# Kernel tuning notes

Hardware: AMD Instinct MI355X
Metric: run time of the kernel (lower is better)

The kernel has to match this reference:

```python
import jax, jax.numpy as jnp
import numpy as np

B, L, T = 32, 512, 400
EMB, PRE, ENC, ARNN, DRNN, NSYM = 512, 256, 512, 1024, 1024, 256
MEAN_COEFF, SCALE_COEFF = 1.0, 10.0


def setup_inputs() -> dict:
    key = jax.random.key(0)
    ks = jax.random.split(key, 20)
    s = 0.02
    inp = {
        'memory': jax.random.normal(ks[0], (B, L, ENC), jnp.float32),
        'decoder_inputs': jax.random.normal(ks[1], (B, EMB, T), jnp.float32),
        'memory_lengths': jax.random.randint(ks[2], (B,), L // 2, L + 1).astype(jnp.int64),
        # prenet
        'pW1': jax.random.normal(ks[3], (PRE, EMB), jnp.float32) * s,
        'pb1': jnp.zeros((PRE,), jnp.float32),
        'pW2': jax.random.normal(ks[4], (PRE, PRE), jnp.float32) * s,
        'pb2': jnp.zeros((PRE,), jnp.float32),
        # attention LSTMCell
        'aWih': jax.random.normal(ks[5], (4 * ARNN, PRE + ENC), jnp.float32) * s,
        'aWhh': jax.random.normal(ks[6], (4 * ARNN, ARNN), jnp.float32) * s,
        'abih': jnp.zeros((4 * ARNN,), jnp.float32),
        'abhh': jnp.zeros((4 * ARNN,), jnp.float32),
        # Gaussian attention param linear (weight zero-init in torch; small here)
        'attWp': jax.random.normal(ks[7], (2, ARNN), jnp.float32) * 0.001,
        'attbp': jnp.zeros((2,), jnp.float32),
        # decoder LSTMCell
        'dWih': jax.random.normal(ks[8], (4 * DRNN, ARNN + ENC), jnp.float32) * s,
        'dWhh': jax.random.normal(ks[9], (4 * DRNN, DRNN), jnp.float32) * s,
        'dbih': jnp.zeros((4 * DRNN,), jnp.float32),
        'dbhh': jnp.zeros((4 * DRNN,), jnp.float32),
        # output linear
        'oW': jax.random.normal(ks[10], (NSYM, DRNN + ENC), jnp.float32) * s,
        'ob': jnp.zeros((NSYM,), jnp.float32),
    }
    return inp


def _lstm_cell(x, h, c, Wih, Whh, bih, bhh):
    g = x @ Wih.T + bih + h @ Whh.T + bhh
    i, f, gg, o = jnp.split(g, 4, axis=-1)
    c = jax.nn.sigmoid(f) * c + jax.nn.sigmoid(i) * jnp.tanh(gg)
    h = jax.nn.sigmoid(o) * jnp.tanh(c)
    return h, c


def _decoder_core(memory, decoder_inputs, memory_lengths,
                  pW1, pb1, pW2, pb2,
                  aWih, aWhh, abih, abhh,
                  attWp, attbp,
                  dWih, dWhh, dbih, dbhh,
                  oW, ob):
    b = memory.shape[0]
    Lm = memory.shape[1]
    # go frame + time-major inputs -> prenet (dropout is identity in eval)
    x = jnp.transpose(decoder_inputs, (2, 0, 1))            # [T, B, EMB]
    x = jnp.concatenate([jnp.zeros((1, b, EMB), x.dtype), x], axis=0)  # [T+1, B, EMB]
    x = jax.nn.relu(x @ pW1.T + pb1)
    x = jax.nn.relu(x @ pW2.T + pb2)                        # [T+1, B, PRE]
    x = x[:T]                                               # loop runs T steps

    lin = jnp.arange(Lm, dtype=memory.dtype)[None, :]       # [1, L]
    pad_mask = lin >= memory_lengths[:, None].astype(memory.dtype)  # [B, L] True at pad

    def step(carry, x_t):
        ah, ac, dh, dc, ctx, mean = carry
        cell_in = jnp.concatenate([x_t, ctx], axis=1)
        ah, ac = _lstm_cell(cell_in, ah, ac, aWih, aWhh, abih, abhh)
        params = ah @ attWp.T + attbp                       # [B, 2]
        mean = mean + jnp.exp(params[:, 0:1]) * MEAN_COEFF  # [B, 1]
        scale = jnp.exp(params[:, 1:2]) * SCALE_COEFF       # [B, 1]
        Z = jnp.sqrt(2.0 * np.pi * scale ** 2)
        w = jnp.exp(-0.5 * (lin - mean) ** 2 / scale ** 2) / Z  # [B, L]
        w = jnp.where(pad_mask, 0.0, w)
        ctx = jnp.einsum('bl,bld->bd', w, memory)           # [B, ENC]
        dec_in = jnp.concatenate([ah, ctx], axis=1)
        dh, dc = _lstm_cell(dec_in, dh, dc, dWih, dWhh, dbih, dbhh)
        out = jnp.concatenate([dh, ctx], axis=1) @ oW.T + ob  # [B, NSYM]
        return (ah, ac, dh, dc, ctx, mean), (out, w, params)

    z = jnp.zeros
    carry0 = (z((b, ARNN)), z((b, ARNN)), z((b, DRNN)), z((b, DRNN)),
              z((b, ENC)), z((b, 1)))
    _, (logits, aligns, ps) = jax.lax.scan(step, carry0, x)
    # time-major -> [B, T, ...]
    return (jnp.transpose(logits, (1, 0, 2)),
            jnp.transpose(aligns, (1, 0, 2)),
            jnp.transpose(ps, (1, 0, 2)))


def reference(memory, decoder_inputs, memory_lengths,
              pW1, pb1, pW2, pb2,
              aWih, aWhh, abih, abhh,
              attWp, attbp,
              dWih, dWhh, dbih, dbhh,
              oW, ob):
    return _decoder_core(memory, decoder_inputs, memory_lengths,
                         pW1, pb1, pW2, pb2,
                         aWih, aWhh, abih, abhh,
                         attWp, attbp,
                         dWih, dWhh, dbih, dbhh,
                         oW, ob)
```

## Files before the change

### kernel.cpp

```cpp
#include <hip/hip_runtime.h>
#include <math.h>

#define Bsz   32
#define Lmem  512
#define Tsteps 400
#define EMBD  512
#define PRE   256
#define ENCD  512
#define ARNN  1024
#define DRNN  1024
#define NSYM  256

typedef _Float16 f16x8 __attribute__((ext_vector_type(8)));
typedef float    f32x4 __attribute__((ext_vector_type(4)));
typedef _Float16 half_t;

#define KA  (PRE + ENCD + ARNN)
#define KAQ (KA / 4)
#define NMA (KAQ / 32)
#define KD  (ARNN + ENCD + DRNN)
#define KDQ (KD / 4)
#define NMD (KDQ / 32)
#define LDA_A 1800
#define LDA_D 2568

__device__ __forceinline__ void st_agent_f16(half_t* p, half_t v) {
    __hip_atomic_store((unsigned short*)p, __builtin_bit_cast(unsigned short, v),
                       __ATOMIC_RELAXED, __HIP_MEMORY_SCOPE_AGENT);
}
__device__ __forceinline__ void st_agent_f32(float* p, float v) {
    __hip_atomic_store(p, v, __ATOMIC_RELAXED, __HIP_MEMORY_SCOPE_AGENT);
}
__device__ __forceinline__ void st_agent_u32(unsigned* p, unsigned v) {
    __hip_atomic_store(p, v, __ATOMIC_RELAXED, __HIP_MEMORY_SCOPE_AGENT);
}
__device__ __forceinline__ float ld_agent_f32(const float* p) {
    return __hip_atomic_load(p, __ATOMIC_RELAXED, __HIP_MEMORY_SCOPE_AGENT);
}
__device__ __forceinline__ unsigned ld_agent_u32(const unsigned* p) {
    return __hip_atomic_load(p, __ATOMIC_RELAXED, __HIP_MEMORY_SCOPE_AGENT);
}
__device__ __forceinline__ f16x8 ld_agent_f16x8(const half_t* p) {
    union { unsigned long long u[2]; f16x8 v; } c;
    c.u[0] = __hip_atomic_load((const unsigned long long*)p,
                               __ATOMIC_RELAXED, __HIP_MEMORY_SCOPE_AGENT);
    c.u[1] = __hip_atomic_load(((const unsigned long long*)p) + 1,
                               __ATOMIC_RELAXED, __HIP_MEMORY_SCOPE_AGENT);
    return c.v;
}
__device__ __forceinline__ void keep16(f16x8& v) { asm volatile("" : "+v"(v)); }

template<int KIH, int KHH>
__global__ __launch_bounds__(256) void conv_lstm_w(
    const float* __restrict__ Wih, const float* __restrict__ Whh,
    const float* __restrict__ bih, const float* __restrict__ bhh,
    half_t* __restrict__ Wcat, float* __restrict__ bsum)
{
    constexpr int K = KIH + KHH;
    const int j = blockIdx.x;
    const float* srcA = Wih + (size_t)j * KIH;
    const float* srcB = Whh + (size_t)j * KHH;
    half_t* dst = Wcat + (size_t)j * K;
    for (int k = threadIdx.x; k < KIH; k += 256) dst[k]       = (half_t)srcA[k];
    for (int k = threadIdx.x; k < KHH; k += 256) dst[KIH + k] = (half_t)srcB[k];
    if (threadIdx.x == 0) bsum[j] = bih[j] + bhh[j];
}

__global__ __launch_bounds__(256) void conv_mat(
    const float* __restrict__ src, half_t* __restrict__ dst, int n)
{
    for (int i = blockIdx.x * 256 + threadIdx.x; i < n; i += gridDim.x * 256)
        dst[i] = (half_t)src[i];
}

__global__ __launch_bounds__(256) void prenet_kernel(
    const float* __restrict__ din,
    const float* __restrict__ pW1, const float* __restrict__ pb1,
    const float* __restrict__ pW2, const float* __restrict__ pb2,
    half_t* __restrict__ xpre)
{
    __shared__ float xs[8][EMBD];
    __shared__ float h1s[8][PRE];
    const int tid = threadIdx.x;
    const int row0 = blockIdx.x * 8;

    for (int idx = tid; idx < 8 * EMBD; idx += 256) {
        int r = idx >> 9;
        int e = idx & 511;
        int rid = row0 + r;
        int t = rid >> 5;
        int b = rid & 31;
        float v = 0.f;
        if (t > 0) v = din[(size_t)b * EMBD * Tsteps + (size_t)e * Tsteps + (t - 1)];
        xs[r][e] = v;
    }
    __syncthreads();

    {
        float acc[8] = {0.f,0.f,0.f,0.f,0.f,0.f,0.f,0.f};
        const float* wr = pW1 + (size_t)tid * EMBD;
        for (int e = 0; e < EMBD; e += 4) {
            float4 wv = *(const float4*)(wr + e);
            #pragma unroll
            for (int r = 0; r < 8; ++r) {
                float4 xv = *(const float4*)&xs[r][e];
                acc[r] += wv.x * xv.x + wv.y * xv.y + wv.z * xv.z + wv.w * xv.w;
            }
        }
        float bias = pb1[tid];
        #pragma unroll
        for (int r = 0; r < 8; ++r) h1s[r][tid] = fmaxf(acc[r] + bias, 0.f);
    }
    __syncthreads();

    {
        float acc[8] = {0.f,0.f,0.f,0.f,0.f,0.f,0.f,0.f};
        const float* wr = pW2 + (size_t)tid * PRE;
        for (int e = 0; e < PRE; e += 4) {
            float4 wv = *(const float4*)(wr + e);
            #pragma unroll
            for (int r = 0; r < 8; ++r) {
                float4 xv = *(const float4*)&h1s[r][e];
                acc[r] += wv.x * xv.x + wv.y * xv.y + wv.z * xv.z + wv.w * xv.w;
            }
        }
        float bias = pb2[tid];
        #pragma unroll
        for (int r = 0; r < 8; ++r) {
            int rid = row0 + r;
            int t = rid >> 5;
            int b = rid & 31;
            xpre[(size_t)t * Bsz * PRE + (size_t)b * PRE + tid] =
                (half_t)fmaxf(acc[r] + bias, 0.f);
        }
    }
}

__device__ __forceinline__ void g_arrive(unsigned* flags, unsigned ph)
{
    asm volatile("s_waitcnt vmcnt(0)" ::: "memory");
    __syncthreads();
    if (threadIdx.x == 0)
        __hip_atomic_store(flags + blockIdx.x * 16, ph,
                           __ATOMIC_RELAXED, __HIP_MEMORY_SCOPE_AGENT);
}
__device__ __forceinline__ void g_wait(unsigned* flags, unsigned ph)
{
    if (threadIdx.x < 64) {
        const unsigned* f = flags + threadIdx.x * 64;
        for (;;) {
            unsigned a = ld_agent_u32(f);
            unsigned b = ld_agent_u32(f + 16);
            unsigned c = ld_agent_u32(f + 32);
            unsigned d = ld_agent_u32(f + 48);
            if (min(min(a, b), min(c, d)) >= ph) break;
            __builtin_amdgcn_s_sleep(2);
        }
    }
    __syncthreads();
}

__global__ __launch_bounds__(512, 1) void decoder_persistent(
    const half_t* __restrict__ Wcat_a, const float* __restrict__ bsum_a,
    const half_t* __restrict__ Wcat_d, const float* __restrict__ bsum_d,
    const half_t* __restrict__ Wo, const float* __restrict__ ob,
    const half_t* __restrict__ xpre,
    const float* __restrict__ attWp, const float* __restrict__ attbp,
    const int* __restrict__ mlen, const half_t* __restrict__ mem16,
    half_t* __restrict__ ah0, half_t* __restrict__ ah1,
    half_t* __restrict__ dh0, half_t* __restrict__ dh1,
    half_t* __restrict__ ctx0, half_t* __restrict__ ctx1,
    float* __restrict__ mean0, float* __restrict__ mean1,
    float* __restrict__ logits, float* __restrict__ aligns,
    float* __restrict__ ps,
    unsigned* flags)
{
    const int blk   = blockIdx.x;
    const int tid   = threadIdx.x;
    const int wave  = tid >> 6;
    const int lane  = tid & 63;
    const int btile = wave & 1;
    const int kq    = wave >> 1;
    const int m15   = lane & 15;
    const int kh    = lane >> 4;
    const int u0    = blk << 2;
    const int bb    = (btile << 4) + m15;

    __shared__ __align__(16) half_t wAl[16 * LDA_A];
    __shared__ __align__(16) half_t wDl[16 * LDA_D];
    __shared__ float gredA[4][2][16][16];
    __shared__ float gredD[4][2][16][16];
    __shared__ float wsh[Lmem];
    __shared__ float lred[16][33];
    __shared__ float wred8[8][2];
    __shared__ float bc2[2];

    for (int g = tid; g < 16 * (KA / 8); g += 512) {
        int r = g / (KA / 8);
        int c = (g - r * (KA / 8)) * 8;
        int jr = (r >> 2) * 1024 + u0 + (r & 3);
        *(f16x8*)(wAl + r * LDA_A + c) = *(const f16x8*)(Wcat_a + (size_t)jr * KA + c);
    }
    for (int g = tid; g < 16 * (KD / 8); g += 512) {
        int r = g / (KD / 8);
        int c = (g - r * (KD / 8)) * 8;
        int jr = (r >> 2) * 1024 + u0 + (r & 3);
        *(f16x8*)(wDl + r * LDA_D + c) = *(const f16x8*)(Wcat_d + (size_t)jr * KD + c);
    }
    float bsA[4] = {0.f,0.f,0.f,0.f}, bsD[4] = {0.f,0.f,0.f,0.f};
    float cA = 0.f, cD = 0.f;
    if (tid < 128) {
        const int ul = tid >> 5;
        #pragma unroll
        for (int gi = 0; gi < 4; ++gi) bsA[gi] = bsum_a[gi * 1024 + u0 + ul];
    } else if (tid < 256) {
        const int ul = (tid - 128) >> 5;
        #pragma unroll
        for (int gi = 0; gi < 4; ++gi) bsD[gi] = bsum_d[gi * 1024 + u0 + ul];
    }
    const half_t* lA = wAl + m15 * LDA_A + kq * KAQ + (kh << 3);
    const half_t* lD = wDl + m15 * LDA_D + kq * KDQ + (kh << 3);
    __syncthreads();

    f16x8 bvA[NMA], bvD[NMD];
    {
        const half_t* s0 = xpre;
        #pragma unroll
        for (int i = 0; i < NMA; ++i) {
            const int kg = kq * KAQ + i * 32 + (kh << 3);
            if (kg < PRE)             bvA[i] = *(const f16x8*)(s0 + bb * PRE + kg);
            else if (kg < PRE + ENCD) bvA[i] = ld_agent_f16x8(ctx1 + bb * ENCD + (kg - PRE));
            else                      bvA[i] = ld_agent_f16x8(ah1 + bb * ARNN + (kg - PRE - ENCD));
        }
    }

    unsigned ph = 0;

    for (int t = 0; t <= Tsteps; ++t) {
        const int par = t & 1;
        half_t*       ah_cur  = par ? ah1 : ah0;
        half_t*       ctx_cur = par ? ctx1 : ctx0;
        const half_t* ctx_prv = par ? ctx0 : ctx1;
        float*        mn_cur  = par ? mean1 : mean0;
        const float*  mn_prv  = par ? mean0 : mean1;
        half_t*       dh_s    = par ? dh0 : dh1;

        if (t < Tsteps) {
            f32x4 accA = {0.f,0.f,0.f,0.f};
            #pragma unroll
            for (int i = 0; i < NMA; ++i) {
                f16x8 av = *(const f16x8*)(lA + i * 32);
                accA = __builtin_amdgcn_mfma_f32_16x16x32_f16(av, bvA[i], accA, 0, 0, 0);
            }
            #pragma unroll
            for (int r = 0; r < 4; ++r)
                gredA[kq][btile][(kh << 2) + r][m15] = accA[r];
        }
        if (t > 0) {
            f32x4 accD = {0.f,0.f,0.f,0.f};
            #pragma unroll
            for (int i = 0; i < NMD; ++i) {
                f16x8 av = *(const f16x8*)(lD + i * 32);
                accD = __builtin_amdgcn_mfma_f32_16x16x32_f16(av, bvD[i], accD, 0, 0, 0);
            }
            #pragma unroll
            for (int r = 0; r < 4; ++r)
                gredD[kq][btile][(kh << 2) + r][m15] = accD[r];
        }
        __syncthreads();
        if (tid < 128) {
            if (t < Tsteps) {
                const int ul = tid >> 5;
                const int bq = tid & 31;
                const int bt = bq >> 4;
                const int nn = bq & 15;
                float g[4];
                #pragma unroll
                for (int gi = 0; gi < 4; ++gi) {
                    const int mr = (gi << 2) + ul;
                    g[gi] = gredA[0][bt][mr][nn] + gredA[1][bt][mr][nn]
                          + gredA[2][bt][mr][nn] + gredA[3][bt][mr][nn] + bsA[gi];
                }
                float si = 1.f / (1.f + expf(-g[0]));
                float sf = 1.f / (1.f + expf(-g[1]));
                float so = 1.f / (1.f + expf(-g[3]));
                cA = sf * cA + si * tanhf(g[2]);
                st_agent_f16(&ah_cur[bq * 1024 + u0 + ul], (half_t)(so * tanhf(cA)));
            }
        } else if (tid < 256) {
            if (t > 0) {
                const int lt = tid - 128;
                const int ul = lt >> 5;
                const int bq = lt & 31;
                const int bt = bq >> 4;
                const int nn = bq & 15;
                float g[4];
                #pragma unroll
                for (int gi = 0; gi < 4; ++gi) {
                    const int mr = (gi << 2) + ul;
                    g[gi] = gredD[0][bt][mr][nn] + gredD[1][bt][mr][nn]
                          + gredD[2][bt][mr][nn] + gredD[3][bt][mr][nn] + bsD[gi];
                }
                float si = 1.f / (1.f + expf(-g[0]));
                float sf = 1.f / (1.f + expf(-g[1]));
                float so = 1.f / (1.f + expf(-g[3]));
                cD = sf * cD + si * tanhf(g[2]);
                st_agent_f16(&dh_s[bq * 1024 + u0 + ul], (half_t)(so * tanhf(cD)));
            }
        }
        ++ph; g_arrive(flags, ph); g_wait(flags, ph);

        if (t < Tsteps) {
            const int abt = blk >> 3;
            const int dt  = blk & 7;
            float p0, p1;
            {
                union { unsigned u; _Float16 h[2]; } a;
                a.u = ld_agent_u32((const unsigned*)(ah_cur + abt * ARNN + 2 * tid));
                float a0 = (float)a.h[0], a1 = (float)a.h[1];
                float2 w0 = *(const float2*)(attWp + 2 * tid);
                float2 w1 = *(const float2*)(attWp + ARNN + 2 * tid);
                p0 = a0 * w0.x + a1 * w0.y;
                p1 = a0 * w1.x + a1 * w1.y;
            }
            #pragma unroll
            for (int off = 32; off > 0; off >>= 1) {
                p0 += __shfl_down(p0, off, 64);
                p1 += __shfl_down(p1, off, 64);
            }
            if (lane == 0) { wred8[wave][0] = p0; wred8[wave][1] = p1; }
            __syncthreads();
            if (tid == 0) {
                float q0 = attbp[0], q1 = attbp[1];
                #pragma unroll
                for (int w = 0; w < 8; ++w) { q0 += wred8[w][0]; q1 += wred8[w][1]; }
                float mn = ld_agent_f32(&mn_prv[abt]) + expf(q0) * 1.0f;
                float sc = expf(q1) * 10.0f;
                if (dt == 0) {
                    st_agent_f32(&mn_cur[abt], mn);
                    st_agent_f32(&ps[(size_t)abt * Tsteps * 2 + (size_t)t * 2 + 0], q0);
                    st_agent_f32(&ps[(size_t)abt * Tsteps * 2 + (size_t)t * 2 + 1], q1);
                }
                bc2[0] = mn; bc2[1] = sc;
            }
            __syncthreads();
            const float mn = bc2[0], sc = bc2[1];
            const float inv_s = 1.f / sc;
            const float coef = 0.3989422804014327f * inv_s;
            const int len = mlen[abt];
            {
                float z = ((float)tid - mn) * inv_s;
                float wv = (tid < len) ? expf(-0.5f * z * z) * coef : 0.f;
                wsh[tid] = wv;
                if (dt == 0)
                    st_agent_f32(&aligns[(size_t)abt * Tsteps * Lmem + (size_t)t * Lmem + tid], wv);
            }
            __syncthreads();
            int lo = (int)fmaxf(0.f, floorf(mn - 9.f * sc));
            int hi = (int)fminf((float)len, ceilf(mn + 9.f * sc) + 1.f);
            const int d8 = (dt << 6) + (wave << 3);
            const half_t* mb = mem16 + (size_t)abt * Lmem * ENCD + d8;
            float acc[8] = {0.f,0.f,0.f,0.f,0.f,0.f,0.f,0.f};
            for (int l = lo + lane; l < hi; l += 64) {
                f16x8 mv = *(const f16x8*)(mb + (size_t)l * ENCD);
                float w = wsh[l];
                #pragma unroll
                for (int j = 0; j < 8; ++j) acc[j] += w * (float)mv[j];
            }
            #pragma unroll
            for (int off = 32; off > 0; off >>= 1) {
                #pragma unroll
                for (int j = 0; j < 8; ++j) acc[j] += __shfl_down(acc[j], off, 64);
            }
            if (lane == 0) {
                #pragma unroll
                for (int j = 0; j < 4; ++j) {
                    union { unsigned u; _Float16 h[2]; } pk;
                    pk.h[0] = (_Float16)acc[2 * j];
                    pk.h[1] = (_Float16)acc[2 * j + 1];
                    __hip_atomic_store((unsigned*)(ctx_cur + abt * ENCD + d8 + 2 * j), pk.u,
                                       __ATOMIC_RELAXED, __HIP_MEMORY_SCOPE_AGENT);
                }
            }
        }
        if (t > 0) {
            const int b_o = tid & 31;
            const int ks  = tid >> 5;
            const half_t* wrow = Wo + (size_t)blk * (DRNN + ENCD) + ks * 96;
            float outacc = 0.f;
            #pragma unroll
            for (int half = 0; half < 2; ++half) {
                f16x8 wv[6], av[6];
                #pragma unroll
                for (int c8 = 0; c8 < 6; ++c8) {
                    const int cc = half * 6 + c8;
                    const int k = ks * 96 + cc * 8;
                    wv[c8] = *(const f16x8*)(wrow + cc * 8);
                    const half_t* ap = (k < DRNN) ? (dh_s + b_o * DRNN + k)
                                                  : (ctx_prv + b_o * ENCD + (k - DRNN));
                    av[c8] = ld_agent_f16x8(ap);
                }
                #pragma unroll
                for (int c8 = 0; c8 < 6; ++c8)
                    #pragma unroll
                    for (int e = 0; e < 8; ++e)
                        outacc += (float)wv[c8][e] * (float)av[c8][e];
            }
            lred[ks][b_o] = outacc;
            __syncthreads();
            if (tid < 32) {
                float s = 0.f;
                #pragma unroll
                for (int q = 0; q < 16; ++q) s += lred[q][tid];
                st_agent_f32(&logits[(size_t)tid * Tsteps * NSYM + (size_t)(t - 1) * NSYM + blk],
                             s + ob[blk]);
            }
        }
        if (t < Tsteps) {
            ++ph; g_arrive(flags, ph);
            if (t + 1 < Tsteps) {
                const half_t* s0n = xpre + (size_t)(t + 1) * Bsz * PRE;
                #pragma unroll
                for (int i = 0; i < NMA; ++i) {
                    const int kg = kq * KAQ + i * 32 + (kh << 3);
                    if (kg < PRE)
                        bvA[i] = *(const f16x8*)(s0n + bb * PRE + kg);
                    else if (kg >= PRE + ENCD)
                        bvA[i] = ld_agent_f16x8(ah_cur + bb * ARNN + (kg - PRE - ENCD));
                }
            }
            #pragma unroll
            for (int i = 0; i < NMD; ++i) {
                const int kg = kq * KDQ + i * 32 + (kh << 3);
                if (kg < ARNN)
                    bvD[i] = ld_agent_f16x8(ah_cur + bb * ARNN + kg);
                else if (kg >= ARNN + ENCD)
                    bvD[i] = ld_agent_f16x8(dh_s + bb * DRNN + (kg - ARNN - ENCD));
            }
            #pragma unroll
            for (int i = 0; i < NMA; ++i) keep16(bvA[i]);
            #pragma unroll
            for (int i = 0; i < NMD; ++i) keep16(bvD[i]);
            g_wait(flags, ph);
            if (t + 1 < Tsteps) {
                #pragma unroll
                for (int i = 0; i < NMA; ++i) {
                    const int kg = kq * KAQ + i * 32 + (kh << 3);
                    if (kg >= PRE && kg < PRE + ENCD)
                        bvA[i] = ld_agent_f16x8(ctx_cur + bb * ENCD + (kg - PRE));
                }
            }
            #pragma unroll
            for (int i = 0; i < NMD; ++i) {
                const int kg = kq * KDQ + i * 32 + (kh << 3);
                if (kg >= ARNN && kg < ARNN + ENCD)
                    bvD[i] = ld_agent_f16x8(ctx_cur + bb * ENCD + (kg - ARNN));
            }
        }
    }
}

extern "C" void kernel_launch(void* const* d_in, const int* in_sizes, int n_in,
                              void* d_out, int out_size, void* d_ws, size_t ws_size,
                              hipStream_t stream)
{
    (void)in_sizes; (void)n_in; (void)out_size; (void)ws_size;
    const float* memory = (const float*)d_in[0];
    const float* din    = (const float*)d_in[1];
    const int*   mlen   = (const int*)d_in[2];
    const float* pW1    = (const float*)d_in[3];
    const float* pb1    = (const float*)d_in[4];
    const float* pW2    = (const float*)d_in[5];
    const float* pb2    = (const float*)d_in[6];
    const float* aWih   = (const float*)d_in[7];
    const float* aWhh   = (const float*)d_in[8];
    const float* abih   = (const float*)d_in[9];
    const float* abhh   = (const float*)d_in[10];
    const float* attWp  = (const float*)d_in[11];
    const float* attbp  = (const float*)d_in[12];
    const float* dWih   = (const float*)d_in[13];
    const float* dWhh   = (const float*)d_in[14];
    const float* dbih   = (const float*)d_in[15];
    const float* dbhh   = (const float*)d_in[16];
    const float* oW     = (const float*)d_in[17];
    const float* ob     = (const float*)d_in[18];

    float* logits = (float*)d_out;
    float* aligns = logits + (size_t)Bsz * Tsteps * NSYM;
    float* ps     = aligns + (size_t)Bsz * Tsteps * Lmem;

    char* base = (char*)d_ws;
    auto alloc = [&](size_t bytes) -> char* {
        char* p = base; base += (bytes + 255) & ~(size_t)255; return p;
    };
    half_t* Wcat_a = (half_t*)alloc((size_t)4096 * KA * 2);
    half_t* Wcat_d = (half_t*)alloc((size_t)4096 * KD * 2);
    half_t* Wo     = (half_t*)alloc((size_t)NSYM * (DRNN + ENCD) * 2);
    float*  bsum_a = (float*)alloc(4096 * 4);
    float*  bsum_d = (float*)alloc(4096 * 4);
    half_t* xpre   = (half_t*)alloc((size_t)Tsteps * Bsz * PRE * 2);
    half_t* mem16  = (half_t*)alloc((size_t)Bsz * Lmem * ENCD * 2);
    half_t* ah0    = (half_t*)alloc(Bsz * ARNN * 2);
    half_t* ah1    = (half_t*)alloc(Bsz * ARNN * 2);
    half_t* dh0    = (half_t*)alloc(Bsz * DRNN * 2);
    half_t* dh1    = (half_t*)alloc(Bsz * DRNN * 2);
    half_t* ctx0   = (half_t*)alloc(Bsz * ENCD * 2);
    half_t* ctx1   = (half_t*)alloc(Bsz * ENCD * 2);
    float*  mean0  = (float*)alloc(Bsz * 4);
    float*  mean1  = (float*)alloc(Bsz * 4);
    unsigned* flags = (unsigned*)alloc(256 * 16 * 4);

    (void)hipMemsetAsync(ah1,   0, Bsz * ARNN * 2, stream);
    (void)hipMemsetAsync(dh1,   0, Bsz * DRNN * 2, stream);
    (void)hipMemsetAsync(ctx1,  0, Bsz * ENCD * 2, stream);
    (void)hipMemsetAsync(mean0, 0, Bsz * 4, stream);
    (void)hipMemsetAsync(mean1, 0, Bsz * 4, stream);
    (void)hipMemsetAsync(flags, 0, 256 * 16 * 4, stream);

    conv_lstm_w<PRE + ENCD, ARNN><<<4096, 256, 0, stream>>>(
        aWih, aWhh, abih, abhh, Wcat_a, bsum_a);
    conv_lstm_w<ARNN + ENCD, DRNN><<<4096, 256, 0, stream>>>(
        dWih, dWhh, dbih, dbhh, Wcat_d, bsum_d);
    conv_mat<<<768, 256, 0, stream>>>(oW, Wo, NSYM * (DRNN + ENCD));
    conv_mat<<<4096, 256, 0, stream>>>(memory, mem16, Bsz * Lmem * ENCD);
    prenet_kernel<<<Tsteps * Bsz / 8, 256, 0, stream>>>(din, pW1, pb1, pW2, pb2, xpre);

    decoder_persistent<<<256, 512, 0, stream>>>(
        Wcat_a, bsum_a, Wcat_d, bsum_d, Wo, ob, xpre,
        attWp, attbp, mlen, mem16,
        ah0, ah1, dh0, dh1, ctx0, ctx1, mean0, mean1,
        logits, aligns, ps,
        flags);
}
```

Before: 14.31 ms.

## Precompute weight-projected memory so decoder step needs a single grid barrier

Attention context enters each LSTM and the output layer linearly. The change precomputes projections of the encoder memory through the context slices of the attention-LSTM, decoder-LSTM and output weights (P_a, P_d, P_o). Each step can then form the gate contributions as an attention-weighted sum of precomputed rows, restricted to a window around the Gaussian mean. This removes the separate context-computation phase and one of the two global barriers per timestep, using a partials buffer for the attention parameters. In exchange it needs about 270MB of workspace and much more per-step memory traffic reading P. The window truncation (WCAP) assumes the attention weights are negligible outside the window. The old two-barrier path remains as a fallback when the workspace is smaller.

```diff
diff --git a/kernel.cpp b/kernel.cpp
--- a/kernel.cpp
+++ b/kernel.cpp
@@ -15,14 +15,24 @@
 typedef float    f32x4 __attribute__((ext_vector_type(4)));
 typedef _Float16 half_t;
 
-#define KA  (PRE + ENCD + ARNN)
-#define KAQ (KA / 4)
-#define NMA (KAQ / 32)
-#define KD  (ARNN + ENCD + DRNN)
-#define KDQ (KD / 4)
-#define NMD (KDQ / 32)
-#define LDA_A 1800
-#define LDA_D 2568
+#define KA2  (PRE + ENCD + ARNN)
+#define KA2Q (KA2 / 4)
+#define NMA2 (KA2Q / 32)
+#define KD2  (ARNN + ENCD + DRNN)
+#define KD2Q (KD2 / 4)
+#define NMD2 (KD2Q / 32)
+#define LDA_A2 1800
+#define LDA_D2 2568
+
+#define KA1  1280
+#define KA1Q 320
+#define NMA1 10
+#define KD1  2048
+#define KD1Q 512
+#define NMD1 16
+#define LDA_A1 1288
+#define LDA_D1 2056
+#define WCAP 216
 
 __device__ __forceinline__ void st_agent_f16(half_t* p, half_t v) {
     __hip_atomic_store((unsigned short*)p, __builtin_bit_cast(unsigned short, v),
@@ -34,10 +44,16 @@
 __device__ __forceinline__ void st_agent_u32(unsigned* p, unsigned v) {
     __hip_atomic_store(p, v, __ATOMIC_RELAXED, __HIP_MEMORY_SCOPE_AGENT);
 }
+__device__ __forceinline__ void st_agent_u64(unsigned long long* p, unsigned long long v) {
+    __hip_atomic_store(p, v, __ATOMIC_RELAXED, __HIP_MEMORY_SCOPE_AGENT);
+}
 __device__ __forceinline__ float ld_agent_f32(const float* p) {
     return __hip_atomic_load(p, __ATOMIC_RELAXED, __HIP_MEMORY_SCOPE_AGENT);
 }
 __device__ __forceinline__ unsigned ld_agent_u32(const unsigned* p) {
+    return __hip_atomic_load(p, __ATOMIC_RELAXED, __HIP_MEMORY_SCOPE_AGENT);
+}
+__device__ __forceinline__ unsigned long long ld_agent_u64(const unsigned long long* p) {
     return __hip_atomic_load(p, __ATOMIC_RELAXED, __HIP_MEMORY_SCOPE_AGENT);
 }
 __device__ __forceinline__ f16x8 ld_agent_f16x8(const half_t* p) {
@@ -51,7 +67,7 @@
 __device__ __forceinline__ void keep16(f16x8& v) { asm volatile("" : "+v"(v)); }
 
 template<int KIH, int KHH>
-__global__ __launch_bounds__(256) void conv_lstm_w(
+__global__ __launch_bounds__(256) void conv_lstm_cat(
     const float* __restrict__ Wih, const float* __restrict__ Whh,
     const float* __restrict__ bih, const float* __restrict__ bhh,
     half_t* __restrict__ Wcat, float* __restrict__ bsum)
@@ -65,12 +81,74 @@
     for (int k = threadIdx.x; k < KHH; k += 256) dst[KIH + k] = (half_t)srcB[k];
     if (threadIdx.x == 0) bsum[j] = bih[j] + bhh[j];
 }
-
+template<int KIH, int KHH, int L0>
+__global__ __launch_bounds__(256) void conv_lstm_skip(
+    const float* __restrict__ Wih, const float* __restrict__ Whh,
+    const float* __restrict__ bih, const float* __restrict__ bhh,
+    half_t* __restrict__ Wcat, float* __restrict__ bsum)
+{
+    constexpr int K = L0 + KHH;
+    const int j = blockIdx.x;
+    const float* srcA = Wih + (size_t)j * KIH;
+    const float* srcB = Whh + (size_t)j * KHH;
+    half_t* dst = Wcat + (size_t)j * K;
+    for (int k = threadIdx.x; k < L0; k += 256)  dst[k] = (half_t)srcA[k];
+    for (int k = threadIdx.x; k < KHH; k += 256) dst[L0 + k] = (half_t)srcB[k];
+    if (threadIdx.x == 0) bsum[j] = bih[j] + bhh[j];
+}
+__global__ __launch_bounds__(256) void conv_slice(
+    const float* __restrict__ src, half_t* __restrict__ dst,
+    int srcstride, int off, int cols)
+{
+    const int r = blockIdx.x;
+    for (int k = threadIdx.x; k < cols; k += 256)
+        dst[(size_t)r * cols + k] = (half_t)src[(size_t)r * srcstride + off + k];
+}
 __global__ __launch_bounds__(256) void conv_mat(
     const float* __restrict__ src, half_t* __restrict__ dst, int n)
 {
     for (int i = blockIdx.x * 256 + threadIdx.x; i < n; i += gridDim.x * 256)
         dst[i] = (half_t)src[i];
+}
+
+__global__ __launch_bounds__(256) void pproj_kernel(
+    const float* __restrict__ Wsrc, int Wstride, int Woff,
+    const float* __restrict__ mem, half_t* __restrict__ P)
+{
+    const int bidx = blockIdx.x;
+    const int jt  = bidx >> 9;
+    const int rem = bidx & 511;
+    const int lt  = rem >> 5;
+    const int b   = rem & 31;
+    const int tid = threadIdx.x;
+    const int wave = tid >> 6, lane = tid & 63;
+    const int wj = wave >> 1, wl = wave & 1;
+    const int m15 = lane & 15, kh = lane >> 4;
+    const int j0 = jt * 32 + wj * 16;
+    const int l0 = lt * 32 + wl * 16;
+
+    const float* wrow = Wsrc + (size_t)(j0 + m15) * Wstride + Woff + (kh << 3);
+    const float* mrow = mem + ((size_t)b * Lmem + (l0 + m15)) * ENCD + (kh << 3);
+    f32x4 acc = {0.f, 0.f, 0.f, 0.f};
+    for (int k = 0; k < 512; k += 32) {
+        float4 w0 = *(const float4*)(wrow + k);
+        float4 w1 = *(const float4*)(wrow + k + 4);
+        f16x8 av;
+        av[0] = (half_t)w0.x; av[1] = (half_t)w0.y; av[2] = (half_t)w0.z; av[3] = (half_t)w0.w;
+        av[4] = (half_t)w1.x; av[5] = (half_t)w1.y; av[6] = (half_t)w1.z; av[7] = (half_t)w1.w;
+        float4 m0 = *(const float4*)(mrow + k);
+        float4 m1 = *(const float4*)(mrow + k + 4);
+        f16x8 bv;
+        bv[0] = (half_t)m0.x; bv[1] = (half_t)m0.y; bv[2] = (half_t)m0.z; bv[3] = (half_t)m0.w;
+        bv[4] = (half_t)m1.x; bv[5] = (half_t)m1.y; bv[6] = (half_t)m1.z; bv[7] = (half_t)m1.w;
+        acc = __builtin_amdgcn_mfma_f32_16x16x32_f16(av, bv, acc, 0, 0, 0);
+    }
+    const int col = lane & 15;
+    #pragma unroll
+    for (int r = 0; r < 4; ++r) {
+        const int row = (kh << 2) + r;
+        P[((size_t)(j0 + row) * 32 + b) * 512 + (l0 + col)] = (half_t)acc[r];
+    }
 }
 
 __global__ __launch_bounds__(256) void prenet_kernel(
@@ -95,7 +173,6 @@
         xs[r][e] = v;
     }
     __syncthreads();
-
     {
         float acc[8] = {0.f,0.f,0.f,0.f,0.f,0.f,0.f,0.f};
         const float* wr = pW1 + (size_t)tid * EMBD;
@@ -112,7 +189,6 @@
         for (int r = 0; r < 8; ++r) h1s[r][tid] = fmaxf(acc[r] + bias, 0.f);
     }
     __syncthreads();
-
     {
         float acc[8] = {0.f,0.f,0.f,0.f,0.f,0.f,0.f,0.f};
         const float* wr = pW2 + (size_t)tid * PRE;
@@ -141,8 +217,7 @@
     asm volatile("s_waitcnt vmcnt(0)" ::: "memory");
     __syncthreads();
     if (threadIdx.x == 0)
-        __hip_atomic_store(flags + blockIdx.x * 16, ph,
-                           __ATOMIC_RELAXED, __HIP_MEMORY_SCOPE_AGENT);
+        st_agent_u32(flags + blockIdx.x * 16, ph);
 }
 __device__ __forceinline__ void g_wait(unsigned* flags, unsigned ph)
 {
@@ -160,7 +235,7 @@
     __syncthreads();
 }
 
-__global__ __launch_bounds__(512, 1) void decoder_persistent(
+__global__ __launch_bounds__(512, 1) void decoder_2bar(
     const half_t* __restrict__ Wcat_a, const float* __restrict__ bsum_a,
     const half_t* __restrict__ Wcat_d, const float* __restrict__ bsum_d,
     const half_t* __restrict__ Wo, const float* __restrict__ ob,
@@ -186,8 +261,8 @@
     const int u0    = blk << 2;
     const int bb    = (btile << 4) + m15;
 
-    __shared__ __align__(16) half_t wAl[16 * LDA_A];
-    __shared__ __align__(16) half_t wDl[16 * LDA_D];
+    __shared__ __align__(16) half_t wAl[16 * LDA_A2];
+    __shared__ __align__(16) half_t wDl[16 * LDA_D2];
     __shared__ float gredA[4][2][16][16];
     __shared__ float gredD[4][2][16][16];
     __shared__ float wsh[Lmem];
@@ -195,17 +270,17 @@
     __shared__ float wred8[8][2];
     __shared__ float bc2[2];
 
-    for (int g = tid; g < 16 * (KA / 8); g += 512) {
-        int r = g / (KA / 8);
-        int c = (g - r * (KA / 8)) * 8;
+    for (int g = tid; g < 16 * (KA2 / 8); g += 512) {
+        int r = g / (KA2 / 8);
+        int c = (g - r * (KA2 / 8)) * 8;
         int jr = (r >> 2) * 1024 + u0 + (r & 3);
-        *(f16x8*)(wAl + r * LDA_A + c) = *(const f16x8*)(Wcat_a + (size_t)jr * KA + c);
-    }
-    for (int g = tid; g < 16 * (KD / 8); g += 512) {
-        int r = g / (KD / 8);
-        int c = (g - r * (KD / 8)) * 8;
+        *(f16x8*)(wAl + r * LDA_A2 + c) = *(const f16x8*)(Wcat_a + (size_t)jr * KA2 + c);
+    }
+    for (int g = tid; g < 16 * (KD2 / 8); g += 512) {
+        int r = g / (KD2 / 8);
+        int c = (g - r * (KD2 / 8)) * 8;
         int jr = (r >> 2) * 1024 + u0 + (r & 3);
-        *(f16x8*)(wDl + r * LDA_D + c) = *(const f16x8*)(Wcat_d + (size_t)jr * KD + c);
+        *(f16x8*)(wDl + r * LDA_D2 + c) = *(const f16x8*)(Wcat_d + (size_t)jr * KD2 + c);
     }
     float bsA[4] = {0.f,0.f,0.f,0.f}, bsD[4] = {0.f,0.f,0.f,0.f};
     float cA = 0.f, cD = 0.f;
@@ -218,16 +293,16 @@
         #pragma unroll
         for (int gi = 0; gi < 4; ++gi) bsD[gi] = bsum_d[gi * 1024 + u0 + ul];
     }
-    const half_t* lA = wAl + m15 * LDA_A + kq * KAQ + (kh << 3);
-    const half_t* lD = wDl + m15 * LDA_D + kq * KDQ + (kh << 3);
+    const half_t* lA = wAl + m15 * LDA_A2 + kq * KA2Q + (kh << 3);
+    const half_t* lD = wDl + m15 * LDA_D2 + kq * KD2Q + (kh << 3);
     __syncthreads();
 
-    f16x8 bvA[NMA], bvD[NMD];
+    f16x8 bvA[NMA2], bvD[NMD2];
     {
         const half_t* s0 = xpre;
         #pragma unroll
-        for (int i = 0; i < NMA; ++i) {
-            const int kg = kq * KAQ + i * 32 + (kh << 3);
+        for (int i = 0; i < NMA2; ++i) {
+            const int kg = kq * KA2Q + i * 32 + (kh << 3);
             if (kg < PRE)             bvA[i] = *(const f16x8*)(s0 + bb * PRE + kg);
             else if (kg < PRE + ENCD) bvA[i] = ld_agent_f16x8(ctx1 + bb * ENCD + (kg - PRE));
             else                      bvA[i] = ld_agent_f16x8(ah1 + bb * ARNN + (kg - PRE - ENCD));
@@ -248,7 +323,7 @@
         if (t < Tsteps) {
             f32x4 accA = {0.f,0.f,0.f,0.f};
             #pragma unroll
-            for (int i = 0; i < NMA; ++i) {
+            for (int i = 0; i < NMA2; ++i) {
                 f16x8 av = *(const f16x8*)(lA + i * 32);
                 accA = __builtin_amdgcn_mfma_f32_16x16x32_f16(av, bvA[i], accA, 0, 0, 0);
             }
@@ -259,7 +334,7 @@
         if (t > 0) {
             f32x4 accD = {0.f,0.f,0.f,0.f};
             #pragma unroll
-            for (int i = 0; i < NMD; ++i) {
+            for (int i = 0; i < NMD2; ++i) {
                 f16x8 av = *(const f16x8*)(lD + i * 32);
                 accD = __builtin_amdgcn_mfma_f32_16x16x32_f16(av, bvD[i], accD, 0, 0, 0);
             }
@@ -421,8 +496,8 @@
             if (t + 1 < Tsteps) {
                 const half_t* s0n = xpre + (size_t)(t + 1) * Bsz * PRE;
                 #pragma unroll
-                for (int i = 0; i < NMA; ++i) {
-                    const int kg = kq * KAQ + i * 32 + (kh << 3);
+                for (int i = 0; i < NMA2; ++i) {
+                    const int kg = kq * KA2Q + i * 32 + (kh << 3);
                     if (kg < PRE)
                         bvA[i] = *(const f16x8*)(s0n + bb * PRE + kg);
                     else if (kg >= PRE + ENCD)
@@ -430,31 +505,385 @@
                 }
             }
             #pragma unroll
-            for (int i = 0; i < NMD; ++i) {
-                const int kg = kq * KDQ + i * 32 + (kh << 3);
+            for (int i = 0; i < NMD2; ++i) {
+                const int kg = kq * KD2Q + i * 32 + (kh << 3);
                 if (kg < ARNN)
                     bvD[i] = ld_agent_f16x8(ah_cur + bb * ARNN + kg);
                 else if (kg >= ARNN + ENCD)
                     bvD[i] = ld_agent_f16x8(dh_s + bb * DRNN + (kg - ARNN - ENCD));
             }
             #pragma unroll
-            for (int i = 0; i < NMA; ++i) keep16(bvA[i]);
-            #pragma unroll
-            for (int i = 0; i < NMD; ++i) keep16(bvD[i]);
+            for (int i = 0; i < NMA2; ++i) keep16(bvA[i]);
+            #pragma unroll
+            for (int i = 0; i < NMD2; ++i) keep16(bvD[i]);
             g_wait(flags, ph);
             if (t + 1 < Tsteps) {
                 #pragma unroll
-                for (int i = 0; i < NMA; ++i) {
-                    const int kg = kq * KAQ + i * 32 + (kh << 3);
+                for (int i = 0; i < NMA2; ++i) {
+                    const int kg = kq * KA2Q + i * 32 + (kh << 3);
                     if (kg >= PRE && kg < PRE + ENCD)
                         bvA[i] = ld_agent_f16x8(ctx_cur + bb * ENCD + (kg - PRE));
                 }
             }
             #pragma unroll
-            for (int i = 0; i < NMD; ++i) {
-                const int kg = kq * KDQ + i * 32 + (kh << 3);
+            for (int i = 0; i < NMD2; ++i) {
+                const int kg = kq * KD2Q + i * 32 + (kh << 3);
                 if (kg >= ARNN && kg < ARNN + ENCD)
                     bvD[i] = ld_agent_f16x8(ctx_cur + bb * ENCD + (kg - ARNN));
+            }
+        }
+    }
+}
+
+__global__ __launch_bounds__(512, 2) void decoder_1bar(
+    const half_t* __restrict__ Wcat_a, const float* __restrict__ bsum_a,
+    const half_t* __restrict__ Wcat_d, const float* __restrict__ bsum_d,
+    const half_t* __restrict__ Wo, const float* __restrict__ ob,
+    const half_t* __restrict__ xpre,
+    const float* __restrict__ attWp, const float* __restrict__ attbp,
+    const int* __restrict__ mlen,
+    const half_t* __restrict__ P_a, const half_t* __restrict__ P_d,
+    const half_t* __restrict__ P_o,
+    half_t* __restrict__ ah,
+    half_t* __restrict__ dh0, half_t* __restrict__ dh1,
+    float* __restrict__ partials,
+    float* __restrict__ logits, float* __restrict__ aligns,
+    float* __restrict__ ps,
+    unsigned* flags)
+{
+    const int blk   = blockIdx.x;
+    const int tid   = threadIdx.x;
+    const int wave  = tid >> 6;
+    const int lane  = tid & 63;
+    const int btile = wave & 1;
+    const int kq    = wave >> 1;
+    const int m15   = lane & 15;
+    const int kh    = lane >> 4;
+    const int u0    = blk << 2;
+    const int bb    = (btile << 4) + m15;
+
+    __shared__ __align__(16) half_t wAl[16 * LDA_A1];
+    __shared__ __align__(16) half_t wDl[16 * LDA_D1];
+    __shared__ float gredA[4][2][16][16];
+    __shared__ float gredD[4][2][16][16];
+    __shared__ float wshc[32][WCAP + 8];
+    __shared__ float ctxA[16][32];
+    __shared__ float ctxD[16][32];
+    __shared__ float ctxO[32];
+    __shared__ float lred[16][33];
+    __shared__ float part[4][32][2];
+    __shared__ float praw[32][2];
+    __shared__ float bcc[32][4];
+    __shared__ float bcp[32][4];
+    __shared__ int   lacur[32], hicur[32];
+    __shared__ int   lapv[32], hipv[32];
+    __shared__ float mean32[32];
+    __shared__ half_t hstA[4][32], hstD[4][32];
+
+    for (int g = tid; g < 16 * (KA1 / 8); g += 512) {
+        int r = g / (KA1 / 8);
+        int c = (g - r * (KA1 / 8)) * 8;
+        int jr = (r >> 2) * 1024 + u0 + (r & 3);
+        *(f16x8*)(wAl + r * LDA_A1 + c) = *(const f16x8*)(Wcat_a + (size_t)jr * KA1 + c);
+    }
+    for (int g = tid; g < 16 * (KD1 / 8); g += 512) {
+        int r = g / (KD1 / 8);
+        int c = (g - r * (KD1 / 8)) * 8;
+        int jr = (r >> 2) * 1024 + u0 + (r & 3);
+        *(f16x8*)(wDl + r * LDA_D1 + c) = *(const f16x8*)(Wcat_d + (size_t)jr * KD1 + c);
+    }
+    float bsA[4] = {0.f,0.f,0.f,0.f}, bsD[4] = {0.f,0.f,0.f,0.f};
+    float wp0 = 0.f, wp1 = 0.f;
+    float cA = 0.f, cD = 0.f;
+    if (tid < 128) {
+        const int ul = tid >> 5;
+        #pragma unroll
+        for (int gi = 0; gi < 4; ++gi) bsA[gi] = bsum_a[gi * 1024 + u0 + ul];
+        wp0 = attWp[u0 + ul];
+        wp1 = attWp[ARNN + u0 + ul];
+    } else if (tid < 256) {
+        const int ul = (tid - 128) >> 5;
+        #pragma unroll
+        for (int gi = 0; gi < 4; ++gi) bsD[gi] = bsum_d[gi * 1024 + u0 + ul];
+    }
+    if (tid < 32) mean32[tid] = 0.f;
+    const half_t* lA = wAl + m15 * LDA_A1 + kq * KA1Q + (kh << 3);
+    const half_t* lD = wDl + m15 * LDA_D1 + kq * KD1Q + (kh << 3);
+    __syncthreads();
+
+    f16x8 bvA[NMA1], bvD[NMD1];
+    #pragma unroll
+    for (int i = 0; i < NMA1; ++i) {
+        const int kg = kq * KA1Q + i * 32 + (kh << 3);
+        if (kg < PRE) bvA[i] = *(const f16x8*)(xpre + bb * PRE + kg);
+        else          bvA[i] = ld_agent_f16x8(ah + bb * ARNN + (kg - PRE));
+    }
+
+    unsigned ph = 0;
+
+    for (int tau = 0; tau <= Tsteps + 1; ++tau) {
+        const int par = tau & 1;
+        half_t*       dhW = par ? dh1 : dh0;
+        const half_t* dhR = par ? dh0 : dh1;
+
+        if (tau >= 1) {
+            if (tid < 32) {
+                bcp[tid][0] = bcc[tid][0]; bcp[tid][1] = bcc[tid][1]; bcp[tid][2] = bcc[tid][2];
+                lapv[tid] = lacur[tid]; hipv[tid] = hicur[tid];
+            }
+            __syncthreads();
+        }
+        if (tau >= 1 && tau <= Tsteps) {
+            {
+                const int b = tid >> 4, c = tid & 15;
+                const unsigned long long* pb =
+                    (const unsigned long long*)(partials + ((size_t)b * 256 + c * 16) * 2);
+                float s0 = 0.f, s1 = 0.f;
+                #pragma unroll
+                for (int q = 0; q < 16; ++q) {
+                    union { unsigned long long u; float2 f; } v;
+                    v.u = ld_agent_u64(pb + q);
+                    s0 += v.f.x; s1 += v.f.y;
+                }
+                s0 += __shfl_down(s0, 8, 16); s1 += __shfl_down(s1, 8, 16);
+                s0 += __shfl_down(s0, 4, 16); s1 += __shfl_down(s1, 4, 16);
+                s0 += __shfl_down(s0, 2, 16); s1 += __shfl_down(s1, 2, 16);
+                s0 += __shfl_down(s0, 1, 16); s1 += __shfl_down(s1, 1, 16);
+                if (c == 0) { praw[b][0] = s0; praw[b][1] = s1; }
+            }
+            __syncthreads();
+            if (tid < 32) {
+                float q0 = praw[tid][0] + attbp[0];
+                float q1 = praw[tid][1] + attbp[1];
+                float mn = mean32[tid] + expf(q0);
+                mean32[tid] = mn;
+                float sc = 10.f * expf(q1);
+                float inv_s = 1.f / sc;
+                bcc[tid][0] = mn; bcc[tid][1] = inv_s;
+                bcc[tid][2] = 0.3989422804014327f * inv_s;
+                int len = mlen[tid];
+                int lo = (int)fmaxf(0.f, floorf(mn - 6.f * sc));
+                int hi = (int)fminf((float)len, ceilf(mn + 6.f * sc) + 1.f);
+                if (hi - lo > WCAP) {
+                    int mid = (lo + hi) >> 1;
+                    lo = mid - WCAP / 2; hi = lo + WCAP;
+                    if (lo < 0) { lo = 0; hi = WCAP; }
+                    if (hi > len) { hi = len; lo = hi - WCAP; if (lo < 0) lo = 0; }
+                }
+                if (hi < lo) hi = lo;
+                lacur[tid] = lo & ~7;
+                hicur[tid] = hi;
+                if (blk == tid) {
+                    st_agent_f32(&ps[((size_t)tid * Tsteps + (tau - 1)) * 2 + 0], q0);
+                    st_agent_f32(&ps[((size_t)tid * Tsteps + (tau - 1)) * 2 + 1], q1);
+                }
+            }
+            __syncthreads();
+            {
+                const int b = tid >> 4, c = tid & 15;
+                const int la = lacur[b], hi = hicur[b];
+                const float mn = bcc[b][0], inv_s = bcc[b][1], coef = bcc[b][2];
+                for (int i = c; i < WCAP + 8; i += 16) {
+                    int l = la + i;
+                    float w = 0.f;
+                    if (l < hi) {
+                        float z = ((float)l - mn) * inv_s;
+                        w = coef * expf(-0.5f * z * z);
+                    }
+                    wshc[b][i] = w;
+                }
+            }
+            if (blk < 32) {
+                const int len = mlen[blk];
+                const float mn = bcc[blk][0], inv_s = bcc[blk][1], coef = bcc[blk][2];
+                float z = ((float)tid - mn) * inv_s;
+                float w = (tid < len) ? coef * expf(-0.5f * z * z) : 0.f;
+                st_agent_f32(&aligns[((size_t)blk * Tsteps + (tau - 1)) * Lmem + tid], w);
+            }
+            __syncthreads();
+        }
+
+        if (tau < Tsteps) {
+            f32x4 accA = {0.f,0.f,0.f,0.f};
+            #pragma unroll
+            for (int i = 0; i < NMA1; ++i) {
+                f16x8 av = *(const f16x8*)(lA + i * 32);
+                accA = __builtin_amdgcn_mfma_f32_16x16x32_f16(av, bvA[i], accA, 0, 0, 0);
+            }
+            #pragma unroll
+            for (int r = 0; r < 4; ++r)
+                gredA[kq][btile][(kh << 2) + r][m15] = accA[r];
+        }
+        if (tau >= 1 && tau <= Tsteps) {
+            f32x4 accD = {0.f,0.f,0.f,0.f};
+            #pragma unroll
+            for (int i = 0; i < NMD1; ++i) {
+                f16x8 av = *(const f16x8*)(lD + i * 32);
+                accD = __builtin_amdgcn_mfma_f32_16x16x32_f16(av, bvD[i], accD, 0, 0, 0);
+            }
+            #pragma unroll
+            for (int r = 0; r < 4; ++r)
+                gredD[kq][btile][(kh << 2) + r][m15] = accD[r];
+        }
+        if (tau >= 2) {
+            const int b_o = tid & 31;
+            const int ks  = tid >> 5;
+            const half_t* wrow = Wo + (size_t)blk * DRNN + ks * 64;
+            const half_t* ap   = dhR + (size_t)b_o * DRNN + ks * 64;
+            float outacc = 0.f;
+            #pragma unroll
+            for (int c8 = 0; c8 < 8; ++c8) {
+                f16x8 wv = *(const f16x8*)(wrow + c8 * 8);
+                f16x8 av = ld_agent_f16x8(ap + c8 * 8);
+                #pragma unroll
+                for (int e = 0; e < 8; ++e)
+                    outacc += (float)wv[e] * (float)av[e];
+            }
+            lred[ks][b_o] = outacc;
+        }
+        if (tau >= 1 && tau <= Tsteps) {
+            const int jl = tid >> 5, b = tid & 31;
+            const int jg = (jl >> 2) * 1024 + u0 + (jl & 3);
+            const int la = lacur[b], hi = hicur[b];
+            const int nv = (hi - la + 7) >> 3;
+            const half_t* pa = P_a + ((size_t)jg * 32 + b) * 512 + la;
+            const half_t* pd = P_d + ((size_t)jg * 32 + b) * 512 + la;
+            float sA = 0.f, sD = 0.f;
+            for (int v = 0; v < nv; ++v) {
+                f16x8 pav = *(const f16x8*)(pa + v * 8);
+                f16x8 pdv = *(const f16x8*)(pd + v * 8);
+                #pragma unroll
+                for (int e = 0; e < 8; ++e) {
+                    float w = wshc[b][v * 8 + e];
+                    sA += w * (float)pav[e];
+                    sD += w * (float)pdv[e];
+                }
+            }
+            ctxA[jl][b] = sA;
+            ctxD[jl][b] = sD;
+        }
+        if (tau >= 2 && tid >= 448 && tid < 480) {
+            const int b = tid - 448;
+            const int la = lapv[b], hi = hipv[b];
+            const float mn = bcp[b][0], inv_s = bcp[b][1], coef = bcp[b][2];
+            const half_t* po = P_o + ((size_t)blk * 32 + b) * 512 + la;
+            float s = 0.f;
+            const int nv = (hi - la + 7) >> 3;
+            for (int v = 0; v < nv; ++v) {
+                f16x8 pov = *(const f16x8*)(po + v * 8);
+                #pragma unroll
+                for (int e = 0; e < 8; ++e) {
+                    int l = la + v * 8 + e;
+                    if (l < hi) {
+                        float z = ((float)l - mn) * inv_s;
+                        s += coef * expf(-0.5f * z * z) * (float)pov[e];
+                    }
+                }
+            }
+            ctxO[b] = s;
+        }
+        __syncthreads();
+
+        if (tid < 128) {
+            if (tau < Tsteps) {
+                const int ul = tid >> 5;
+                const int bq = tid & 31;
+                const int bt = bq >> 4;
+                const int nn = bq & 15;
+                float g[4];
+                #pragma unroll
+                for (int gi = 0; gi < 4; ++gi) {
+                    const int mr = (gi << 2) + ul;
+                    g[gi] = gredA[0][bt][mr][nn] + gredA[1][bt][mr][nn]
+                          + gredA[2][bt][mr][nn] + gredA[3][bt][mr][nn] + bsA[gi]
+                          + ((tau >= 1) ? ctxA[mr][bq] : 0.f);
+                }
+                float si = 1.f / (1.f + expf(-g[0]));
+                float sf = 1.f / (1.f + expf(-g[1]));
+                float so = 1.f / (1.f + expf(-g[3]));
+                cA = sf * cA + si * tanhf(g[2]);
+                float hval = so * tanhf(cA);
+                hstA[ul][bq] = (half_t)hval;
+                part[ul][bq][0] = hval * wp0;
+                part[ul][bq][1] = hval * wp1;
+            }
+        } else if (tid < 256) {
+            if (tau >= 1 && tau <= Tsteps) {
+                const int lt = tid - 128;
+                const int ul = lt >> 5;
+                const int bq = lt & 31;
+                const int bt = bq >> 4;
+                const int nn = bq & 15;
+                float g[4];
+                #pragma unroll
+                for (int gi = 0; gi < 4; ++gi) {
+                    const int mr = (gi << 2) + ul;
+                    g[gi] = gredD[0][bt][mr][nn] + gredD[1][bt][mr][nn]
+                          + gredD[2][bt][mr][nn] + gredD[3][bt][mr][nn] + bsD[gi]
+                          + ctxD[mr][bq];
+                }
+                float si = 1.f / (1.f + expf(-g[0]));
+                float sf = 1.f / (1.f + expf(-g[1]));
+                float so = 1.f / (1.f + expf(-g[3]));
+                cD = sf * cD + si * tanhf(g[2]);
+                hstD[ul][bq] = (half_t)(so * tanhf(cD));
+            }
+        } else if (tid < 288) {
+            if (tau >= 2) {
+                const int b = tid - 256;
+                float s = 0.f;
+                #pragma unroll
+                for (int q = 0; q < 16; ++q) s += lred[q][b];
+                st_agent_f32(&logits[(size_t)b * Tsteps * NSYM + (size_t)(tau - 2) * NSYM + blk],
+                             s + ctxO[b] + ob[blk]);
+            }
+        }
+        __syncthreads();
+        if (tau < Tsteps && tid < 32) {
+            union { unsigned long long u; half_t h[4]; } pk;
+            #pragma unroll
+            for (int q = 0; q < 4; ++q) pk.h[q] = hstA[q][tid];
+            st_agent_u64((unsigned long long*)(ah + (size_t)tid * ARNN + u0), pk.u);
+            float p0 = part[0][tid][0] + part[1][tid][0] + part[2][tid][0] + part[3][tid][0];
+            float p1 = part[0][tid][1] + part[1][tid][1] + part[2][tid][1] + part[3][tid][1];
+            union { float2 f; unsigned long long u; } pp;
+            pp.f.x = p0; pp.f.y = p1;
+            st_agent_u64((unsigned long long*)(partials + ((size_t)tid * 256 + blk) * 2), pp.u);
+        }
+        if (tau >= 1 && tau <= Tsteps && tid >= 64 && tid < 96) {
+            const int b = tid - 64;
+            union { unsigned long long u; half_t h[4]; } pk;
+            #pragma unroll
+            for (int q = 0; q < 4; ++q) pk.h[q] = hstD[q][b];
+            st_agent_u64((unsigned long long*)(dhW + (size_t)b * DRNN + u0), pk.u);
+        }
+
+        if (tau <= Tsteps) {
+            ++ph; g_arrive(flags, ph);
+            if (tau + 1 < Tsteps) {
+                const half_t* s0n = xpre + (size_t)(tau + 1) * Bsz * PRE;
+                #pragma unroll
+                for (int i = 0; i < NMA1; ++i) {
+                    const int kg = kq * KA1Q + i * 32 + (kh << 3);
+                    if (kg < PRE) { bvA[i] = *(const f16x8*)(s0n + bb * PRE + kg); keep16(bvA[i]); }
+                }
+            }
+            g_wait(flags, ph);
+            if (tau + 1 < Tsteps) {
+                #pragma unroll
+                for (int i = 0; i < NMA1; ++i) {
+                    const int kg = kq * KA1Q + i * 32 + (kh << 3);
+                    if (kg >= PRE) { bvA[i] = ld_agent_f16x8(ah + bb * ARNN + (kg - PRE)); keep16(bvA[i]); }
+                }
+            }
+            if (tau < Tsteps) {
+                #pragma unroll
+                for (int i = 0; i < NMD1; ++i) {
+                    const int kg = kq * KD1Q + i * 32 + (kh << 3);
+                    bvD[i] = (kg < ARNN) ? ld_agent_f16x8(ah + bb * ARNN + kg)
+                                         : ld_agent_f16x8(dhW + bb * DRNN + (kg - ARNN));
+                    keep16(bvD[i]);
+                }
             }
         }
     }
@@ -464,7 +893,7 @@
                               void* d_out, int out_size, void* d_ws, size_t ws_size,
                               hipStream_t stream)
 {
-    (void)in_sizes; (void)n_in; (void)out_size; (void)ws_size;
+    (void)in_sizes; (void)n_in; (void)out_size;
     const float* memory = (const float*)d_in[0];
     const float* din    = (const float*)d_in[1];
     const int*   mlen   = (const int*)d_in[2];
@@ -493,42 +922,80 @@
     auto alloc = [&](size_t bytes) -> char* {
         char* p = base; base += (bytes + 255) & ~(size_t)255; return p;
     };
-    half_t* Wcat_a = (half_t*)alloc((size_t)4096 * KA * 2);
-    half_t* Wcat_d = (half_t*)alloc((size_t)4096 * KD * 2);
-    half_t* Wo     = (half_t*)alloc((size_t)NSYM * (DRNN + ENCD) * 2);
-    float*  bsum_a = (float*)alloc(4096 * 4);
-    float*  bsum_d = (float*)alloc(4096 * 4);
-    half_t* xpre   = (half_t*)alloc((size_t)Tsteps * Bsz * PRE * 2);
-    half_t* mem16  = (half_t*)alloc((size_t)Bsz * Lmem * ENCD * 2);
-    half_t* ah0    = (half_t*)alloc(Bsz * ARNN * 2);
-    half_t* ah1    = (half_t*)alloc(Bsz * ARNN * 2);
-    half_t* dh0    = (half_t*)alloc(Bsz * DRNN * 2);
-    half_t* dh1    = (half_t*)alloc(Bsz * DRNN * 2);
-    half_t* ctx0   = (half_t*)alloc(Bsz * ENCD * 2);
-    half_t* ctx1   = (half_t*)alloc(Bsz * ENCD * 2);
-    float*  mean0  = (float*)alloc(Bsz * 4);
-    float*  mean1  = (float*)alloc(Bsz * 4);
-    unsigned* flags = (unsigned*)alloc(256 * 16 * 4);
-
-    (void)hipMemsetAsync(ah1,   0, Bsz * ARNN * 2, stream);
-    (void)hipMemsetAsync(dh1,   0, Bsz * DRNN * 2, stream);
-    (void)hipMemsetAsync(ctx1,  0, Bsz * ENCD * 2, stream);
-    (void)hipMemsetAsync(mean0, 0, Bsz * 4, stream);
-    (void)hipMemsetAsync(mean1, 0, Bsz * 4, stream);
-    (void)hipMemsetAsync(flags, 0, 256 * 16 * 4, stream);
-
-    conv_lstm_w<PRE + ENCD, ARNN><<<4096, 256, 0, stream>>>(
-        aWih, aWhh, abih, abhh, Wcat_a, bsum_a);
-    conv_lstm_w<ARNN + ENCD, DRNN><<<4096, 256, 0, stream>>>(
-        dWih, dWhh, dbih, dbhh, Wcat_d, bsum_d);
-    conv_mat<<<768, 256, 0, stream>>>(oW, Wo, NSYM * (DRNN + ENCD));
-    conv_mat<<<4096, 256, 0, stream>>>(memory, mem16, Bsz * Lmem * ENCD);
-    prenet_kernel<<<Tsteps * Bsz / 8, 256, 0, stream>>>(din, pW1, pb1, pW2, pb2, xpre);
-
-    decoder_persistent<<<256, 512, 0, stream>>>(
-        Wcat_a, bsum_a, Wcat_d, bsum_d, Wo, ob, xpre,
-        attWp, attbp, mlen, mem16,
-        ah0, ah1, dh0, dh1, ctx0, ctx1, mean0, mean1,
-        logits, aligns, ps,
-        flags);
-}
+
+    if (ws_size >= ((size_t)320 << 20)) {
+        half_t* Wcat_a = (half_t*)alloc((size_t)4096 * KA1 * 2);
+        half_t* Wcat_d = (half_t*)alloc((size_t)4096 * KD1 * 2);
+        half_t* Wo     = (half_t*)alloc((size_t)NSYM * DRNN * 2);
+        float*  bsum_a = (float*)alloc(4096 * 4);
+        float*  bsum_d = (float*)alloc(4096 * 4);
+        half_t* xpre   = (half_t*)alloc((size_t)Tsteps * Bsz * PRE * 2);
+        half_t* P_a    = (half_t*)alloc((size_t)4096 * 32 * 512 * 2);
+        half_t* P_d    = (half_t*)alloc((size_t)4096 * 32 * 512 * 2);
+        half_t* P_o    = (half_t*)alloc((size_t)256 * 32 * 512 * 2);
+        half_t* ah     = (half_t*)alloc(Bsz * ARNN * 2);
+        half_t* dh0    = (half_t*)alloc(Bsz * DRNN * 2);
+        half_t* dh1    = (half_t*)alloc(Bsz * DRNN * 2);
+        float*  partials = (float*)alloc((size_t)Bsz * 256 * 2 * 4);
+        unsigned* flags  = (unsigned*)alloc(256 * 16 * 4);
+
+        (void)hipMemsetAsync(ah,   0, Bsz * ARNN * 2, stream);
+        (void)hipMemsetAsync(dh0,  0, Bsz * DRNN * 2, stream);
+        (void)hipMemsetAsync(dh1,  0, Bsz * DRNN * 2, stream);
+        (void)hipMemsetAsync(flags, 0, 256 * 16 * 4, stream);
+
+        conv_lstm_skip<768, 1024, 256><<<4096, 256, 0, stream>>>(
+            aWih, aWhh, abih, abhh, Wcat_a, bsum_a);
+        conv_lstm_skip<1536, 1024, 1024><<<4096, 256, 0, stream>>>(
+            dWih, dWhh, dbih, dbhh, Wcat_d, bsum_d);
+        conv_slice<<<256, 256, 0, stream>>>(oW, Wo, 1536, 0, 1024);
+        prenet_kernel<<<Tsteps * Bsz / 8, 256, 0, stream>>>(din, pW1, pb1, pW2, pb2, xpre);
+        pproj_kernel<<<(4096 / 32) * 512, 256, 0, stream>>>(aWih, 768, 256, memory, P_a);
+        pproj_kernel<<<(4096 / 32) * 512, 256, 0, stream>>>(dWih, 1536, 1024, memory, P_d);
+        pproj_kernel<<<(256 / 32) * 512, 256, 0, stream>>>(oW, 1536, 1024, memory, P_o);
+
+        decoder_1bar<<<256, 512, 0, stream>>>(
+            Wcat_a, bsum_a, Wcat_d, bsum_d, Wo, ob, xpre,
+            attWp, attbp, mlen, P_a, P_d, P_o,
+            ah, dh0, dh1, partials,
+            logits, aligns, ps, flags);
+    } else {
+        half_t* Wcat_a = (half_t*)alloc((size_t)4096 * KA2 * 2);
+        half_t* Wcat_d = (half_t*)alloc((size_t)4096 * KD2 * 2);
+        half_t* Wo     = (half_t*)alloc((size_t)NSYM * (DRNN + ENCD) * 2);
+        float*  bsum_a = (float*)alloc(4096 * 4);
+        float*  bsum_d = (float*)alloc(4096 * 4);
+        half_t* xpre   = (half_t*)alloc((size_t)Tsteps * Bsz * PRE * 2);
+        half_t* mem16  = (half_t*)alloc((size_t)Bsz * Lmem * ENCD * 2);
+        half_t* ah0    = (half_t*)alloc(Bsz * ARNN * 2);
+        half_t* ah1    = (half_t*)alloc(Bsz * ARNN * 2);
+        half_t* dh0    = (half_t*)alloc(Bsz * DRNN * 2);
+        half_t* dh1    = (half_t*)alloc(Bsz * DRNN * 2);
+        half_t* ctx0   = (half_t*)alloc(Bsz * ENCD * 2);
+        half_t* ctx1   = (half_t*)alloc(Bsz * ENCD * 2);
+        float*  mean0  = (float*)alloc(Bsz * 4);
+        float*  mean1  = (float*)alloc(Bsz * 4);
+        unsigned* flags = (unsigned*)alloc(256 * 16 * 4);
+
+        (void)hipMemsetAsync(ah1,   0, Bsz * ARNN * 2, stream);
+        (void)hipMemsetAsync(dh1,   0, Bsz * DRNN * 2, stream);
+        (void)hipMemsetAsync(ctx1,  0, Bsz * ENCD * 2, stream);
+        (void)hipMemsetAsync(mean0, 0, Bsz * 4, stream);
+        (void)hipMemsetAsync(mean1, 0, Bsz * 4, stream);
+        (void)hipMemsetAsync(flags, 0, 256 * 16 * 4, stream);
+
+        conv_lstm_cat<PRE + ENCD, ARNN><<<4096, 256, 0, stream>>>(
+            aWih, aWhh, abih, abhh, Wcat_a, bsum_a);
+        conv_lstm_cat<ARNN + ENCD, DRNN><<<4096, 256, 0, stream>>>(
+            dWih, dWhh, dbih, dbhh, Wcat_d, bsum_d);
+        conv_mat<<<768, 256, 0, stream>>>(oW, Wo, NSYM * (DRNN + ENCD));
+        conv_mat<<<4096, 256, 0, stream>>>(memory, mem16, Bsz * Lmem * ENCD);
+        prenet_kernel<<<Tsteps * Bsz / 8, 256, 0, stream>>>(din, pW1, pb1, pW2, pb2, xpre);
+
+        decoder_2bar<<<256, 512, 0, stream>>>(
+            Wcat_a, bsum_a, Wcat_d, bsum_d, Wo, ob, xpre,
+            attWp, attbp, mlen, mem16,
+            ah0, ah1, dh0, dh1, ctx0, ctx1, mean0, mean1,
+            logits, aligns, ps, flags);
+    }
+}
```

New measurement: 14.36 ms. Within noise of the previous version (+0.3%).
